# Kernel tuning notes

Measured on AMD Instinct MI355X. Metric: run time of the kernel, lower is better.

## Reference

```python
import jax, jax.numpy as jnp
import numpy as np

B, IN, COND, H, LAT, E, GH = 8192, 256, 1024, 1024, 128, 6, 64
INP = LAT + COND      # decoder layer0 input size = 1152
INTER = LAT + H       # decoder layer1/2 input size = 1152


def setup_inputs() -> dict:
    key = jax.random.key(0)
    ks = jax.random.split(key, 30)
    n = lambda k, shape, s=0.02: jax.random.normal(k, shape, dtype=jnp.float32) * s
    return {
        'x': jax.random.normal(ks[0], (B, IN), dtype=jnp.float32),
        'y': jax.random.normal(ks[1], (B, COND), dtype=jnp.float32),
        'eps': jax.random.normal(ks[2], (B, LAT), dtype=jnp.float32),
        # encoder: layer k input = prev_dim + IN (x is re-concatenated each layer)
        'enc_w0': n(ks[3], (IN + COND + IN, H)), 'enc_b0': jnp.zeros((H,), jnp.float32),
        'enc_w1': n(ks[4], (H + IN, H)),         'enc_b1': jnp.zeros((H,), jnp.float32),
        'mu_w': n(ks[5], (H, LAT)),  'mu_b': jnp.zeros((LAT,), jnp.float32),
        'lv_w': n(ks[6], (H, LAT)),  'lv_b': jnp.zeros((LAT,), jnp.float32),
        # gating network (input = latent + cond)
        'g_w0': n(ks[7], (INP, GH)), 'g_b0': jnp.zeros((GH,), jnp.float32),
        'g_w1': n(ks[8], (GH, GH)),  'g_b1': jnp.zeros((GH,), jnp.float32),
        'g_w2': n(ks[9], (GH, E)),   'g_b2': jnp.zeros((E,), jnp.float32),
        # expert weights [E, in, out] and biases [E, out] (bias init 0.01 as in source)
        'exp_w0': n(ks[10], (E, INP, H)),   'exp_b0': jnp.full((E, H), 0.01, jnp.float32),
        'exp_w1': n(ks[11], (E, INTER, H)), 'exp_b1': jnp.full((E, H), 0.01, jnp.float32),
        'exp_w2': n(ks[12], (E, INTER, IN)), 'exp_b2': jnp.full((E, IN), 0.01, jnp.float32),
    }


def _forward(x, y, eps, enc_w0, enc_b0, enc_w1, enc_b1, mu_w, mu_b, lv_w, lv_b,
             g_w0, g_b0, g_w1, g_b1, g_w2, g_b2,
             exp_w0, exp_b0, exp_w1, exp_b1, exp_w2, exp_b2):
    elu = jax.nn.elu
    # --- Encoder ---
    h = jnp.concatenate([x, y], axis=1)
    h = elu(jnp.concatenate([h, x], axis=1) @ enc_w0 + enc_b0)
    h = elu(jnp.concatenate([h, x], axis=1) @ enc_w1 + enc_b1)
    mu = h @ mu_w + mu_b
    logvar = h @ lv_w + lv_b
    # --- Reparameterize (eps passed explicitly for determinism) ---
    z = mu + eps * jnp.exp(0.5 * logvar)
    # --- MixedDecoder ---
    g = jnp.concatenate([z, y], axis=1)
    g = elu(g @ g_w0 + g_b0)
    g = elu(g @ g_w1 + g_b1)
    coeff = jax.nn.softmax(g @ g_w2 + g_b2, axis=1)  # [B, E]
    layer_out = y
    for W, bb, act in ((exp_w0, exp_b0, True), (exp_w1, exp_b1, True), (exp_w2, exp_b2, False)):
        inp = jnp.concatenate([z, layer_out], axis=1)  # [B, I]
        # fused mixture-of-experts projection: avoids materializing per-sample [B,I,O] weight
        out = coeff @ bb + jnp.einsum('be,bi,eio->bo', coeff, inp, W)
        layer_out = elu(out) if act else out
    return layer_out, mu, logvar


def reference(x, y, eps, enc_w0, enc_b0, enc_w1, enc_b1, mu_w, mu_b, lv_w, lv_b,
              g_w0, g_b0, g_w1, g_b1, g_w2, g_b2,
              exp_w0, exp_b0, exp_w1, exp_b1, exp_w2, exp_b2):
    return _forward(x, y, eps, enc_w0, enc_b0, enc_w1, enc_b1, mu_w, mu_b, lv_w, lv_b,
                    g_w0, g_b0, g_w1, g_b1, g_w2, g_b2,
                    exp_w0, exp_b0, exp_w1, exp_b1, exp_w2, exp_b2)
```

## Files before the change

### kernel.cpp

```cpp
#include <hip/hip_runtime.h>
#include <hip/hip_bf16.h>
#include <cstddef>

using u16 = unsigned short;
using short8 = __attribute__((ext_vector_type(8))) short;
using f32x4 = __attribute__((ext_vector_type(4))) float;

constexpr int B_   = 8192;
constexpr int IN_  = 256;
constexpr int COND_= 1024;
constexpr int H_   = 1024;
constexpr int LAT_ = 128;
constexpr int NE_  = 6;
constexpr int GH_  = 64;
constexpr int INP_ = 1152;
constexpr int K0_  = 1536;
constexpr int K1_  = 1280;

constexpr int BK = 64;

typedef const __attribute__((address_space(1))) void gv_t;
typedef __attribute__((address_space(3))) void lv_t;
#define GLDS(g, l) __builtin_amdgcn_global_load_lds((gv_t*)(g), (lv_t*)(l), 16, 0, 0)

__device__ __forceinline__ u16 f2b(float f) {
  __hip_bfloat16 h = __float2bfloat16(f);
  return *reinterpret_cast<u16*>(&h);
}
__device__ __forceinline__ float elu1(float x) { return x > 0.f ? x : (__expf(x) - 1.f); }

__global__ void k_transpose(const float* __restrict__ in, u16* __restrict__ out,
                            int R, int C, long inStride, long outStride) {
  __shared__ float t[32][33];
  const float* ip = in + (long)blockIdx.z * inStride;
  u16* op = out + (long)blockIdx.z * outStride;
  int c0 = blockIdx.x * 32, r0 = blockIdx.y * 32;
  int tx = threadIdx.x, ty = threadIdx.y;
#pragma unroll
  for (int i = 0; i < 4; i++) {
    int r = r0 + ty + i * 8, c = c0 + tx;
    if (r < R && c < C) t[ty + i * 8][tx] = ip[(long)r * C + c];
  }
  __syncthreads();
#pragma unroll
  for (int i = 0; i < 4; i++) {
    int c = c0 + ty + i * 8, r = r0 + tx;
    if (r < R && c < C) op[(long)c * R + r] = f2b(t[tx][ty + i * 8]);
  }
}

__global__ void k_prep(const float* __restrict__ x, const float* __restrict__ y,
                       u16* __restrict__ A0, u16* __restrict__ A1) {
  long idx = (long)blockIdx.x * blockDim.x + threadIdx.x;
  long n0 = (long)B_ * K0_;
  if (idx < n0) {
    int b = (int)(idx / K0_), c = (int)(idx % K0_);
    float v;
    if (c < IN_)            v = x[(long)b * IN_ + c];
    else if (c < IN_+COND_) v = y[(long)b * COND_ + (c - IN_)];
    else                    v = x[(long)b * IN_ + (c - IN_ - COND_)];
    A0[idx] = f2b(v);
  } else {
    long j = idx - n0;
    if (j < (long)B_ * IN_) {
      int b = (int)(j / IN_), c = (int)(j % IN_);
      A1[(long)b * K1_ + H_ + c] = f2b(x[(long)b * IN_ + c]);
    }
  }
}

__global__ void k_z(const float* __restrict__ mu, const float* __restrict__ lv,
                    const float* __restrict__ eps, const float* __restrict__ y,
                    u16* __restrict__ ZY, u16* __restrict__ D1, u16* __restrict__ D2) {
  long idx = (long)blockIdx.x * blockDim.x + threadIdx.x;
  if (idx >= (long)B_ * INP_) return;
  int b = (int)(idx / INP_), c = (int)(idx % INP_);
  if (c < LAT_) {
    long o = (long)b * LAT_ + c;
    float z = mu[o] + eps[o] * __expf(0.5f * lv[o]);
    u16 zb = f2b(z);
    ZY[idx] = zb; D1[idx] = zb; D2[idx] = zb;
  } else {
    ZY[idx] = f2b(y[(long)b * COND_ + (c - LAT_)]);
  }
}

__global__ __launch_bounds__(256) void k_gate(const float* __restrict__ G1,
    const float* __restrict__ w1, const float* __restrict__ b1,
    const float* __restrict__ w2, const float* __restrict__ b2,
    float* __restrict__ coeff) {
  __shared__ float W1[64][65];
  __shared__ float W2[64][8];
  __shared__ float B1[64], B2[8];
  int tid = threadIdx.x;
  for (int i = tid; i < 64 * 64; i += 256) W1[i >> 6][i & 63] = w1[i];
  for (int i = tid; i < 64 * 6; i += 256) W2[i / 6][i % 6] = w2[i];
  if (tid < 64) B1[tid] = b1[tid];
  if (tid < 8)  B2[tid] = (tid < 6) ? b2[tid] : 0.f;
  __syncthreads();
  int row = blockIdx.x * 256 + tid;
  const float* gr = G1 + (long)row * GH_;
  float g[64];
#pragma unroll
  for (int i = 0; i < 16; i++) {
    float4 v = *(const float4*)(gr + i * 4);
    g[i*4] = v.x; g[i*4+1] = v.y; g[i*4+2] = v.z; g[i*4+3] = v.w;
  }
  float lg[6];
#pragma unroll
  for (int e = 0; e < 6; e++) lg[e] = B2[e];
  for (int n = 0; n < 64; n++) {
    float s = B1[n];
#pragma unroll
    for (int k = 0; k < 64; k++) s += g[k] * W1[k][n];
    s = elu1(s);
#pragma unroll
    for (int e = 0; e < 6; e++) lg[e] += s * W2[n][e];
  }
  float m = lg[0];
#pragma unroll
  for (int e = 1; e < 6; e++) m = fmaxf(m, lg[e]);
  float p[6], sum = 0.f;
#pragma unroll
  for (int e = 0; e < 6; e++) { p[e] = __expf(lg[e] - m); sum += p[e]; }
  float inv = 1.f / sum;
#pragma unroll
  for (int e = 0; e < 6; e++) coeff[(long)row * 6 + e] = p[e] * inv;
}

template<int KSTEPS, int E, bool MOE>
__global__ __launch_bounds__(512, 2) void k_gemm8(
    const u16* __restrict__ A,
    const u16* __restrict__ WT,
    const float* __restrict__ bias,
    const float* __restrict__ coeff,
    int N,
    u16* __restrict__ outH, int ldo)
{
  constexpr int KK = KSTEPS * BK;
  constexpr int T = E * KSTEPS;
  __shared__ __align__(16) u16 As[3][256][BK];
  __shared__ __align__(16) u16 Bs[3][128][BK];
  __shared__ float Cf[MOE ? 256 : 1][8];

  const int tid = threadIdx.x;
  const int lane = tid & 63, w = tid >> 6;
  const int wr = w >> 1, wc = w & 1;
  const int lin = blockIdx.x + blockIdx.y * gridDim.x;
  const int rb  = (lin & 7) * 4 + ((lin >> 3) & 3);
  const int cp  = lin >> 5;
  const int brow = rb * 256, bcol = cp * 128;
  const int lr = lane & 15, hi = lane >> 4;
  const int lk = hi * 8;
  const int xsw = (lr & 7) << 3;

  if (MOE) {
    if (tid < 256) {
#pragma unroll
      for (int e2 = 0; e2 < 8; e2++)
        Cf[tid][e2] = (e2 < 6) ? coeff[(long)(brow + tid) * 6 + e2] : 0.f;
    }
    __syncthreads();
  }

  f32x4 acc[4][4];
#pragma unroll
  for (int m = 0; m < 4; m++)
#pragma unroll
    for (int n = 0; n < 4; n++)
#pragma unroll
      for (int r = 0; r < 4; r++) acc[m][n][r] = 0.f;
  f32x4 pacc[MOE ? 4 : 1][MOE ? 4 : 1];
  if constexpr (MOE) {
#pragma unroll
    for (int m = 0; m < 4; m++)
#pragma unroll
      for (int n = 0; n < 4; n++)
#pragma unroll
        for (int r = 0; r < 4; r++) pacc[m][n][r] = 0.f;
  }

  const int srow = w * 8 + (lane >> 3);
  const int sdst = (lane & 7) * 8;
  const int ssrc = ((lane & 7) ^ ((lane >> 3) & 7)) * 8;
  const u16* Asrc = A + (long)(brow + srow) * KK + ssrc;
  const u16* Bsrc = WT + (long)(bcol + srow) * KK + ssrc;

  auto STAGE = [&](int t2, int buf) {
    const int e2 = (E == 1) ? 0 : (t2 / KSTEPS);
    int k2 = (E == 1) ? t2 : (t2 % KSTEPS);
    if (E > 1 && (e2 & 1)) k2 = KSTEPS - 1 - k2;
    const u16* ap = Asrc + k2 * BK;
    const u16* bp = Bsrc + (long)e2 * ((long)N * KK) + k2 * BK;
#pragma unroll
    for (int i = 0; i < 4; i++)
      GLDS(ap + (long)(i * 64) * KK, &As[buf][i * 64 + srow][sdst]);
#pragma unroll
    for (int i = 0; i < 2; i++)
      GLDS(bp + (long)(i * 64) * KK, &Bs[buf][i * 64 + srow][sdst]);
  };

  STAGE(0, 0);
  STAGE(1, 1);

  for (int t = 0; t < T; ++t) {
    if (t + 1 < T) asm volatile("s_waitcnt vmcnt(6)" ::: "memory");
    else           asm volatile("s_waitcnt vmcnt(0)" ::: "memory");
    asm volatile("s_barrier" ::: "memory");
    if (t + 2 < T) STAGE(t + 2, (t + 2) % 3);
    const int cur = t % 3;
#pragma unroll
    for (int kk = 0; kk < BK; kk += 32) {
      short8 af[4], bfr[4];
      const int cc = (kk + lk) ^ xsw;
#pragma unroll
      for (int m = 0; m < 4; m++)
        af[m] = *(const short8*)&As[cur][wr * 64 + m * 16 + lr][cc];
#pragma unroll
      for (int n = 0; n < 4; n++)
        bfr[n] = *(const short8*)&Bs[cur][wc * 64 + n * 16 + lr][cc];
      __builtin_amdgcn_s_setprio(1);
#pragma unroll
      for (int m = 0; m < 4; m++)
#pragma unroll
        for (int n = 0; n < 4; n++) {
          if constexpr (MOE)
            pacc[m][n] = __builtin_amdgcn_mfma_f32_16x16x32_bf16(af[m], bfr[n], pacc[m][n], 0, 0, 0);
          else
            acc[m][n] = __builtin_amdgcn_mfma_f32_16x16x32_bf16(af[m], bfr[n], acc[m][n], 0, 0, 0);
        }
      __builtin_amdgcn_s_setprio(0);
    }
    if constexpr (MOE) {
      if ((t + 1) % KSTEPS == 0) {
        const int e = t / KSTEPS;
#pragma unroll
        for (int m = 0; m < 4; m++)
#pragma unroll
          for (int r = 0; r < 4; r++) {
            float c = Cf[wr * 64 + m * 16 + hi * 4 + r][e];
#pragma unroll
            for (int n = 0; n < 4; n++) acc[m][n][r] += c * pacc[m][n][r];
          }
        if (t + 1 < T) {
#pragma unroll
          for (int m = 0; m < 4; m++)
#pragma unroll
            for (int n = 0; n < 4; n++)
#pragma unroll
              for (int r = 0; r < 4; r++) pacc[m][n][r] = 0.f;
        }
      }
    }
  }

#pragma unroll
  for (int m = 0; m < 4; m++)
#pragma unroll
    for (int n = 0; n < 4; n++) {
      const int col = bcol + wc * 64 + n * 16 + lr;
#pragma unroll
      for (int r = 0; r < 4; r++) {
        const int rowl = wr * 64 + m * 16 + hi * 4 + r;
        const long row = brow + rowl;
        float v = acc[m][n][r];
        if constexpr (MOE) {
          float bv = 0.f;
#pragma unroll
          for (int e = 0; e < 6; e++) bv += Cf[rowl][e] * bias[(long)e * N + col];
          v += bv;
        } else {
          v += bias[col];
        }
        v = elu1(v);
        outH[row * (long)ldo + col] = f2b(v);
      }
    }
}

template<int MREP, bool MOE>
__global__ __launch_bounds__(256, 2) void k_gemm(
    const u16* __restrict__ A, int lda,
    const u16* __restrict__ WT, long wstride,
    const float* __restrict__ bias,
    const float* __restrict__ coeff,
    int N, int K, int E,
    u16* __restrict__ outH, float* __restrict__ outF, float* __restrict__ outF2,
    int ldo, int splitcol, const float* __restrict__ bias2, int act)
{
  constexpr int BMt = 32 * MREP;
  __shared__ __align__(16) u16 As[2][BMt][BK];
  __shared__ __align__(16) u16 Bs[2][128][BK];
  __shared__ float Cf[MOE ? BMt : 1][8];

  const int tid = threadIdx.x;
  const int lane = tid & 63, w = tid >> 6;
  const int wr = w >> 1, wc = w & 1;
  const int brow = blockIdx.x * BMt, bcol = blockIdx.y * 128;
  const int lr = lane & 15, hi = lane >> 4;
  const int lk = hi * 8;
  const int xsw = (lr & 7) << 3;

  if (MOE && tid < BMt) {
#pragma unroll
    for (int e2 = 0; e2 < 8; e2++)
      Cf[tid][e2] = (e2 < 6) ? coeff[(long)(brow + tid) * 6 + e2] : 0.f;
  }

  f32x4 acc[MREP][4];
#pragma unroll
  for (int m = 0; m < MREP; m++)
#pragma unroll
    for (int n = 0; n < 4; n++)
#pragma unroll
      for (int r = 0; r < 4; r++) acc[m][n][r] = 0.f;

  const int srow = w * 8 + (lane >> 3);
  const int sdst = (lane & 7) * 8;
  const int ssrc = ((lane & 7) ^ ((lane >> 3) & 7)) * 8;
  const u16* Asrc = A + (long)(brow + srow) * lda + ssrc;
  const u16* Bsrc = WT + (long)(bcol + srow) * K + ssrc;
  const int KSTEPS = K / BK;

  int cur = 0;
#pragma unroll
  for (int i = 0; i < BMt / 32; i++)
    GLDS(Asrc + (long)(i * 32) * lda, &As[0][i * 32 + srow][sdst]);
#pragma unroll
  for (int i = 0; i < 4; i++)
    GLDS(Bsrc + (long)(i * 32) * K, &Bs[0][i * 32 + srow][sdst]);

  for (int e = 0; e < E; ++e) {
    f32x4 pacc[MREP][4];
    if constexpr (MOE) {
#pragma unroll
      for (int m = 0; m < MREP; m++)
#pragma unroll
        for (int n = 0; n < 4; n++)
#pragma unroll
          for (int r = 0; r < 4; r++) pacc[m][n][r] = 0.f;
    }

    for (int kt = 0; kt < KSTEPS; ++kt) {
      __syncthreads();
      int ne = e, nk = kt + 1;
      if (nk == KSTEPS) { nk = 0; ne = e + 1; }
      if (ne < E) {
        const u16* ap = Asrc + (long)nk * BK;
        const u16* bp = Bsrc + (long)ne * wstride + (long)nk * BK;
#pragma unroll
        for (int i = 0; i < BMt / 32; i++)
          GLDS(ap + (long)(i * 32) * lda, &As[cur ^ 1][i * 32 + srow][sdst]);
#pragma unroll
        for (int i = 0; i < 4; i++)
          GLDS(bp + (long)(i * 32) * K, &Bs[cur ^ 1][i * 32 + srow][sdst]);
      }
#pragma unroll
      for (int kk = 0; kk < BK; kk += 32) {
        short8 af[MREP], bfr[4];
        const int cc = (kk + lk) ^ xsw;
#pragma unroll
        for (int m = 0; m < MREP; m++)
          af[m] = *(const short8*)&As[cur][wr * (16 * MREP) + m * 16 + lr][cc];
#pragma unroll
        for (int n = 0; n < 4; n++)
          bfr[n] = *(const short8*)&Bs[cur][wc * 64 + n * 16 + lr][cc];
#pragma unroll
        for (int m = 0; m < MREP; m++)
#pragma unroll
          for (int n = 0; n < 4; n++) {
            if constexpr (MOE)
              pacc[m][n] = __builtin_amdgcn_mfma_f32_16x16x32_bf16(af[m], bfr[n], pacc[m][n], 0, 0, 0);
            else
              acc[m][n] = __builtin_amdgcn_mfma_f32_16x16x32_bf16(af[m], bfr[n], acc[m][n], 0, 0, 0);
          }
      }
      cur ^= 1;
    }
    if constexpr (MOE) {
#pragma unroll
      for (int m = 0; m < MREP; m++)
#pragma unroll
        for (int r = 0; r < 4; r++) {
          float c = Cf[wr * (16 * MREP) + m * 16 + hi * 4 + r][e];
#pragma unroll
          for (int n = 0; n < 4; n++) acc[m][n][r] += c * pacc[m][n][r];
        }
    }
  }

#pragma unroll
  for (int m = 0; m < MREP; m++)
#pragma unroll
    for (int n = 0; n < 4; n++) {
      int col = bcol + wc * 64 + n * 16 + lr;
      if (col >= N) continue;
#pragma unroll
      for (int r = 0; r < 4; r++) {
        int rowl = wr * (16 * MREP) + m * 16 + hi * 4 + r;
        long row = brow + rowl;
        float v = acc[m][n][r];
        if constexpr (MOE) {
          float bv = 0.f;
#pragma unroll
          for (int e = 0; e < 6; e++) bv += Cf[rowl][e] * bias[(long)e * N + col];
          v += bv;
        } else {
          v += (col < splitcol) ? bias[col] : bias2[col - splitcol];
        }
        if (act) v = elu1(v);
        if (outH) outH[row * ldo + col] = f2b(v);
        else if (col < splitcol) outF[row * ldo + col] = v;
        else outF2[row * ldo + (col - splitcol)] = v;
      }
    }
}

extern "C" void kernel_launch(void* const* d_in, const int* in_sizes, int n_in,
                              void* d_out, int out_size, void* d_ws, size_t ws_size,
                              hipStream_t stream) {
  (void)in_sizes; (void)out_size;
  if (n_in < 23) return;
  const float* x      = (const float*)d_in[0];
  const float* y      = (const float*)d_in[1];
  const float* eps    = (const float*)d_in[2];
  const float* enc_w0 = (const float*)d_in[3];
  const float* enc_b0 = (const float*)d_in[4];
  const float* enc_w1 = (const float*)d_in[5];
  const float* enc_b1 = (const float*)d_in[6];
  const float* mu_w   = (const float*)d_in[7];
  const float* mu_b   = (const float*)d_in[8];
  const float* lv_w   = (const float*)d_in[9];
  const float* lv_b   = (const float*)d_in[10];
  const float* g_w0   = (const float*)d_in[11];
  const float* g_b0   = (const float*)d_in[12];
  const float* g_w1   = (const float*)d_in[13];
  const float* g_b1   = (const float*)d_in[14];
  const float* g_w2   = (const float*)d_in[15];
  const float* g_b2   = (const float*)d_in[16];
  const float* exp_w0 = (const float*)d_in[17];
  const float* exp_b0 = (const float*)d_in[18];
  const float* exp_w1 = (const float*)d_in[19];
  const float* exp_b1 = (const float*)d_in[20];
  const float* exp_w2 = (const float*)d_in[21];
  const float* exp_b2 = (const float*)d_in[22];

  char* ws = (char*)d_ws;
  size_t off = 0;
  auto alloc = [&](size_t bytes) -> void* {
    void* p = ws + off; off += (bytes + 255) & ~(size_t)255; return p;
  };
  u16* A0     = (u16*)alloc((size_t)B_ * K0_ * 2);
  u16* A1     = (u16*)alloc((size_t)B_ * K1_ * 2);
  u16* H2     = (u16*)alloc((size_t)B_ * H_ * 2);
  u16* ZY     = (u16*)alloc((size_t)B_ * INP_ * 2);
  u16* encw0T = (u16*)alloc((size_t)K0_ * H_ * 2);
  u16* encw1T = (u16*)alloc((size_t)K1_ * H_ * 2);
  u16* mulvT  = (u16*)alloc((size_t)256 * H_ * 2);
  u16* gw0T   = (u16*)alloc((size_t)GH_ * INP_ * 2);
  u16* ew0T   = (u16*)alloc((size_t)NE_ * H_ * INP_ * 2);
  if (ws_size < off) return;

  u16* D1 = A0;
  u16* D2 = A1;
  float* G1    = (float*)H2;
  float* COEFF = (float*)((char*)H2 + (size_t)B_ * GH_ * 4);
  u16* ew2T = (u16*)((char*)H2 + (size_t)4 * 1024 * 1024);
  u16* ew1T = ZY;

  float* outO = (float*)d_out;
  float* muO  = outO + (size_t)B_ * IN_;
  float* lvO  = muO + (size_t)B_ * LAT_;

  dim3 tb(32, 8);
  k_transpose<<<dim3(32, 48), tb, 0, stream>>>(enc_w0, encw0T, K0_, H_, 0, 0);
  k_transpose<<<dim3(32, 40), tb, 0, stream>>>(enc_w1, encw1T, K1_, H_, 0, 0);
  k_transpose<<<dim3(4, 32),  tb, 0, stream>>>(mu_w, mulvT, H_, LAT_, 0, 0);
  k_transpose<<<dim3(4, 32),  tb, 0, stream>>>(lv_w, mulvT + (size_t)LAT_ * H_, H_, LAT_, 0, 0);
  k_transpose<<<dim3(2, 36),  tb, 0, stream>>>(g_w0, gw0T, INP_, GH_, 0, 0);
  k_transpose<<<dim3(32, 36, NE_), tb, 0, stream>>>(exp_w0, ew0T, INP_, H_,
                                                    (long)INP_ * H_, (long)INP_ * H_);
  long npr = (long)B_ * K0_ + (long)B_ * IN_;
  k_prep<<<(int)((npr + 255) / 256), 256, 0, stream>>>(x, y, A0, A1);

  k_gemm8<K0_ / BK, 1, false><<<dim3(32, 8), 512, 0, stream>>>(A0, encw0T, enc_b0,
      nullptr, H_, A1, K1_);
  k_gemm8<K1_ / BK, 1, false><<<dim3(32, 8), 512, 0, stream>>>(A1, encw1T, enc_b1,
      nullptr, H_, H2, H_);
  k_gemm<2, false><<<dim3(B_ / 64, 2), 256, 0, stream>>>(H2, H_, mulvT, 0, mu_b, nullptr,
      256, H_, 1, nullptr, muO, lvO, LAT_, LAT_, lv_b, 0);

  k_transpose<<<dim3(8, 36, NE_), tb, 0, stream>>>(exp_w2, ew2T, INP_, IN_,
                                                   (long)INP_ * IN_, (long)INP_ * IN_);
  long nz = (long)B_ * INP_;
  k_z<<<(int)((nz + 255) / 256), 256, 0, stream>>>(muO, lvO, eps, y, ZY, D1, D2);

  k_gemm<2, false><<<dim3(B_ / 64, 1), 256, 0, stream>>>(ZY, INP_, gw0T, 0, g_b0, nullptr,
      GH_, INP_, 1, nullptr, G1, nullptr, GH_, GH_, nullptr, 1);
  k_gate<<<B_ / 256, 256, 0, stream>>>(G1, g_w1, g_b1, g_w2, g_b2, COEFF);

  k_gemm8<INP_ / BK, NE_, true><<<dim3(32, 8), 512, 0, stream>>>(ZY, ew0T, exp_b0,
      COEFF, H_, D1 + LAT_, INP_);
  k_transpose<<<dim3(32, 36, NE_), tb, 0, stream>>>(exp_w1, ew1T, INP_, H_,
                                                    (long)INP_ * H_, (long)INP_ * H_);
  k_gemm8<INP_ / BK, NE_, true><<<dim3(32, 8), 512, 0, stream>>>(D1, ew1T, exp_b1,
      COEFF, H_, D2 + LAT_, INP_);
  k_gemm<2, true><<<dim3(B_ / 64, 2), 256, 0, stream>>>(D2, INP_, ew2T, (long)IN_ * INP_,
      exp_b2, COEFF, IN_, INP_, NE_, nullptr, outO, nullptr, IN_, IN_, nullptr, 0);
}
```

Baseline: 639.4 us.

## Split K-tile staging into halves interleaved with MFMA phases

Restructures the GEMM main loop into two explicit half-tile phases. Each phase reads its LDS fragments, issues half of the next tile's global-to-LDS loads, then runs its MFMAs, with barriers between phases. The aim is to spread memory traffic across the compute and so hide load latency better. The cost is more barriers per iteration and fragile vmcnt accounting.

```diff
diff --git a/kernel.cpp b/kernel.cpp
--- a/kernel.cpp
+++ b/kernel.cpp
@@ -186,39 +186,38 @@
   const u16* Asrc = A + (long)(brow + srow) * KK + ssrc;
   const u16* Bsrc = WT + (long)(bcol + srow) * KK + ssrc;
 
-  auto STAGE = [&](int t2, int buf) {
+  auto STAGE_H = [&](int t2, int buf, int h) {
     const int e2 = (E == 1) ? 0 : (t2 / KSTEPS);
     int k2 = (E == 1) ? t2 : (t2 % KSTEPS);
     if (E > 1 && (e2 & 1)) k2 = KSTEPS - 1 - k2;
-    const u16* ap = Asrc + k2 * BK;
-    const u16* bp = Bsrc + (long)e2 * ((long)N * KK) + k2 * BK;
-#pragma unroll
-    for (int i = 0; i < 4; i++)
-      GLDS(ap + (long)(i * 64) * KK, &As[buf][i * 64 + srow][sdst]);
-#pragma unroll
-    for (int i = 0; i < 2; i++)
-      GLDS(bp + (long)(i * 64) * KK, &Bs[buf][i * 64 + srow][sdst]);
+    const u16* ap = Asrc + (long)k2 * BK;
+    const u16* bp = Bsrc + (long)e2 * ((long)N * KK) + (long)k2 * BK;
+    GLDS(ap + (long)((h * 2 + 0) * 64) * KK, &As[buf][(h * 2 + 0) * 64 + srow][sdst]);
+    GLDS(ap + (long)((h * 2 + 1) * 64) * KK, &As[buf][(h * 2 + 1) * 64 + srow][sdst]);
+    GLDS(bp + (long)(h * 64) * KK,           &Bs[buf][h * 64 + srow][sdst]);
   };
 
-  STAGE(0, 0);
-  STAGE(1, 1);
+  STAGE_H(0, 0, 0); STAGE_H(0, 0, 1);
+  STAGE_H(1, 1, 0); STAGE_H(1, 1, 1);
+  asm volatile("s_waitcnt vmcnt(6)" ::: "memory");
+  asm volatile("s_barrier" ::: "memory");
 
   for (int t = 0; t < T; ++t) {
-    if (t + 1 < T) asm volatile("s_waitcnt vmcnt(6)" ::: "memory");
-    else           asm volatile("s_waitcnt vmcnt(0)" ::: "memory");
-    asm volatile("s_barrier" ::: "memory");
-    if (t + 2 < T) STAGE(t + 2, (t + 2) % 3);
     const int cur = t % 3;
-#pragma unroll
-    for (int kk = 0; kk < BK; kk += 32) {
+    const int nbuf = (t + 2) % 3;
+    const bool do_stage = (t + 2 < T);
+
+    {
       short8 af[4], bfr[4];
-      const int cc = (kk + lk) ^ xsw;
+      const int cc = lk ^ xsw;
 #pragma unroll
       for (int m = 0; m < 4; m++)
         af[m] = *(const short8*)&As[cur][wr * 64 + m * 16 + lr][cc];
 #pragma unroll
       for (int n = 0; n < 4; n++)
         bfr[n] = *(const short8*)&Bs[cur][wc * 64 + n * 16 + lr][cc];
+      if (do_stage) STAGE_H(t + 2, nbuf, 0);
+      asm volatile("s_barrier" ::: "memory");
       __builtin_amdgcn_s_setprio(1);
 #pragma unroll
       for (int m = 0; m < 4; m++)
@@ -230,7 +229,38 @@
             acc[m][n] = __builtin_amdgcn_mfma_f32_16x16x32_bf16(af[m], bfr[n], acc[m][n], 0, 0, 0);
         }
       __builtin_amdgcn_s_setprio(0);
-    }
+      asm volatile("s_barrier" ::: "memory");
+    }
+
+    {
+      short8 af[4], bfr[4];
+      const int cc = (32 + lk) ^ xsw;
+#pragma unroll
+      for (int m = 0; m < 4; m++)
+        af[m] = *(const short8*)&As[cur][wr * 64 + m * 16 + lr][cc];
+#pragma unroll
+      for (int n = 0; n < 4; n++)
+        bfr[n] = *(const short8*)&Bs[cur][wc * 64 + n * 16 + lr][cc];
+      if (do_stage) STAGE_H(t + 2, nbuf, 1);
+      asm volatile("s_barrier" ::: "memory");
+      __builtin_amdgcn_s_setprio(1);
+#pragma unroll
+      for (int m = 0; m < 4; m++)
+#pragma unroll
+        for (int n = 0; n < 4; n++) {
+          if constexpr (MOE)
+            pacc[m][n] = __builtin_amdgcn_mfma_f32_16x16x32_bf16(af[m], bfr[n], pacc[m][n], 0, 0, 0);
+          else
+            acc[m][n] = __builtin_amdgcn_mfma_f32_16x16x32_bf16(af[m], bfr[n], acc[m][n], 0, 0, 0);
+        }
+      __builtin_amdgcn_s_setprio(0);
+      if (t + 1 < T) {
+        if (do_stage) asm volatile("s_waitcnt vmcnt(6)" ::: "memory");
+        else          asm volatile("s_waitcnt vmcnt(0)" ::: "memory");
+      }
+      asm volatile("s_barrier" ::: "memory");
+    }
+
     if constexpr (MOE) {
       if ((t + 1) % KSTEPS == 0) {
         const int e = t / KSTEPS;
```

New measurement: 564.5 us. 11.7% less time.

## Shrink main GEMM to 128x128 tiles with BK=32 and 4 waves

Applied to the files above, without the earlier changes.

Replaces the 256x128 tile, 8-wave, BK=64 GEMM with a 128x128 tile, 4-wave, BK=32 kernel on a 64x8 grid. The LDS swizzle becomes a 4-chunk XOR pattern. The loop is reordered so LDS fragment reads happen before the next stage's global-to-LDS loads are issued, with a single barrier per step. Smaller tiles double the block count and cut LDS use, which may raise occupancy. In exchange each block reuses loaded tiles less and needs twice as many K iterations and barriers.

```diff
diff --git a/kernel.cpp b/kernel.cpp
--- a/kernel.cpp
+++ b/kernel.cpp
@@ -129,7 +129,7 @@
 }
 
 template<int KSTEPS, int E, bool MOE>
-__global__ __launch_bounds__(512, 2) void k_gemm8(
+__global__ __launch_bounds__(256, 2) void k_g4(
     const u16* __restrict__ A,
     const u16* __restrict__ WT,
     const float* __restrict__ bias,
@@ -137,28 +137,27 @@
     int N,
     u16* __restrict__ outH, int ldo)
 {
-  constexpr int KK = KSTEPS * BK;
+  constexpr int KK = KSTEPS * 32;
   constexpr int T = E * KSTEPS;
-  __shared__ __align__(16) u16 As[3][256][BK];
-  __shared__ __align__(16) u16 Bs[3][128][BK];
-  __shared__ float Cf[MOE ? 256 : 1][8];
+  __shared__ __align__(16) u16 As[3][128][32];
+  __shared__ __align__(16) u16 Bs[3][128][32];
+  __shared__ float Cf[MOE ? 128 : 1][6];
 
   const int tid = threadIdx.x;
   const int lane = tid & 63, w = tid >> 6;
   const int wr = w >> 1, wc = w & 1;
   const int lin = blockIdx.x + blockIdx.y * gridDim.x;
-  const int rb  = (lin & 7) * 4 + ((lin >> 3) & 3);
-  const int cp  = lin >> 5;
-  const int brow = rb * 256, bcol = cp * 128;
+  const int rb  = (lin & 7) * 8 + ((lin >> 3) & 7);
+  const int cp  = lin >> 6;
+  const int brow = rb * 128, bcol = cp * 128;
   const int lr = lane & 15, hi = lane >> 4;
-  const int lk = hi * 8;
-  const int xsw = (lr & 7) << 3;
+  const int xsw3 = (lr & 3) ^ ((lr >> 2) & 3);
 
   if (MOE) {
-    if (tid < 256) {
-#pragma unroll
-      for (int e2 = 0; e2 < 8; e2++)
-        Cf[tid][e2] = (e2 < 6) ? coeff[(long)(brow + tid) * 6 + e2] : 0.f;
+    if (tid < 128) {
+#pragma unroll
+      for (int e2 = 0; e2 < 6; e2++)
+        Cf[tid][e2] = coeff[(long)(brow + tid) * 6 + e2];
     }
     __syncthreads();
   }
@@ -180,9 +179,9 @@
         for (int r = 0; r < 4; r++) pacc[m][n][r] = 0.f;
   }
 
-  const int srow = w * 8 + (lane >> 3);
-  const int sdst = (lane & 7) * 8;
-  const int ssrc = ((lane & 7) ^ ((lane >> 3) & 7)) * 8;
+  const int srow = w * 16 + (lane >> 2);
+  const int sdst = (lane & 3) * 8;
+  const int ssrc = (((lane & 3) ^ ((lane >> 2) & 3) ^ ((lane >> 4) & 3))) * 8;
   const u16* Asrc = A + (long)(brow + srow) * KK + ssrc;
   const u16* Bsrc = WT + (long)(bcol + srow) * KK + ssrc;
 
@@ -190,47 +189,47 @@
     const int e2 = (E == 1) ? 0 : (t2 / KSTEPS);
     int k2 = (E == 1) ? t2 : (t2 % KSTEPS);
     if (E > 1 && (e2 & 1)) k2 = KSTEPS - 1 - k2;
-    const u16* ap = Asrc + k2 * BK;
-    const u16* bp = Bsrc + (long)e2 * ((long)N * KK) + k2 * BK;
-#pragma unroll
-    for (int i = 0; i < 4; i++)
-      GLDS(ap + (long)(i * 64) * KK, &As[buf][i * 64 + srow][sdst]);
-#pragma unroll
-    for (int i = 0; i < 2; i++)
-      GLDS(bp + (long)(i * 64) * KK, &Bs[buf][i * 64 + srow][sdst]);
+    const u16* ap = Asrc + (long)k2 * 32;
+    const u16* bp = Bsrc + (long)e2 * ((long)N * KK) + (long)k2 * 32;
+    GLDS(ap,                  &As[buf][srow][sdst]);
+    GLDS(ap + (long)64 * KK,  &As[buf][64 + srow][sdst]);
+    GLDS(bp,                  &Bs[buf][srow][sdst]);
+    GLDS(bp + (long)64 * KK,  &Bs[buf][64 + srow][sdst]);
   };
 
   STAGE(0, 0);
   STAGE(1, 1);
+  asm volatile("s_waitcnt vmcnt(4)" ::: "memory");
+  asm volatile("s_barrier" ::: "memory");
 
   for (int t = 0; t < T; ++t) {
-    if (t + 1 < T) asm volatile("s_waitcnt vmcnt(6)" ::: "memory");
-    else           asm volatile("s_waitcnt vmcnt(0)" ::: "memory");
+    const int cur = t % 3;
+    short8 af[4], bfr[4];
+    const int cc = (hi ^ xsw3) << 3;
+#pragma unroll
+    for (int m = 0; m < 4; m++)
+      af[m] = *(const short8*)&As[cur][wr * 64 + m * 16 + lr][cc];
+#pragma unroll
+    for (int n = 0; n < 4; n++)
+      bfr[n] = *(const short8*)&Bs[cur][wc * 64 + n * 16 + lr][cc];
+    if (t + 2 < T) STAGE(t + 2, (t + 2) % 3);
+    __builtin_amdgcn_s_setprio(1);
+#pragma unroll
+    for (int m = 0; m < 4; m++)
+#pragma unroll
+      for (int n = 0; n < 4; n++) {
+        if constexpr (MOE)
+          pacc[m][n] = __builtin_amdgcn_mfma_f32_16x16x32_bf16(af[m], bfr[n], pacc[m][n], 0, 0, 0);
+        else
+          acc[m][n] = __builtin_amdgcn_mfma_f32_16x16x32_bf16(af[m], bfr[n], acc[m][n], 0, 0, 0);
+      }
+    __builtin_amdgcn_s_setprio(0);
+    if (t + 1 < T) {
+      if (t + 2 < T) asm volatile("s_waitcnt vmcnt(4)" ::: "memory");
+      else           asm volatile("s_waitcnt vmcnt(0)" ::: "memory");
+    }
     asm volatile("s_barrier" ::: "memory");
-    if (t + 2 < T) STAGE(t + 2, (t + 2) % 3);
-    const int cur = t % 3;
-#pragma unroll
-    for (int kk = 0; kk < BK; kk += 32) {
-      short8 af[4], bfr[4];
-      const int cc = (kk + lk) ^ xsw;
-#pragma unroll
-      for (int m = 0; m < 4; m++)
-        af[m] = *(const short8*)&As[cur][wr * 64 + m * 16 + lr][cc];
-#pragma unroll
-      for (int n = 0; n < 4; n++)
-        bfr[n] = *(const short8*)&Bs[cur][wc * 64 + n * 16 + lr][cc];
-      __builtin_amdgcn_s_setprio(1);
-#pragma unroll
-      for (int m = 0; m < 4; m++)
-#pragma unroll
-        for (int n = 0; n < 4; n++) {
-          if constexpr (MOE)
-            pacc[m][n] = __builtin_amdgcn_mfma_f32_16x16x32_bf16(af[m], bfr[n], pacc[m][n], 0, 0, 0);
-          else
-            acc[m][n] = __builtin_amdgcn_mfma_f32_16x16x32_bf16(af[m], bfr[n], acc[m][n], 0, 0, 0);
-        }
-      __builtin_amdgcn_s_setprio(0);
-    }
+
     if constexpr (MOE) {
       if ((t + 1) % KSTEPS == 0) {
         const int e = t / KSTEPS;
@@ -483,9 +482,9 @@
   long npr = (long)B_ * K0_ + (long)B_ * IN_;
   k_prep<<<(int)((npr + 255) / 256), 256, 0, stream>>>(x, y, A0, A1);
 
-  k_gemm8<K0_ / BK, 1, false><<<dim3(32, 8), 512, 0, stream>>>(A0, encw0T, enc_b0,
+  k_g4<K0_ / 32, 1, false><<<dim3(64, 8), 256, 0, stream>>>(A0, encw0T, enc_b0,
       nullptr, H_, A1, K1_);
-  k_gemm8<K1_ / BK, 1, false><<<dim3(32, 8), 512, 0, stream>>>(A1, encw1T, enc_b1,
+  k_g4<K1_ / 32, 1, false><<<dim3(64, 8), 256, 0, stream>>>(A1, encw1T, enc_b1,
       nullptr, H_, H2, H_);
   k_gemm<2, false><<<dim3(B_ / 64, 2), 256, 0, stream>>>(H2, H_, mulvT, 0, mu_b, nullptr,
       256, H_, 1, nullptr, muO, lvO, LAT_, LAT_, lv_b, 0);
@@ -499,11 +498,11 @@
       GH_, INP_, 1, nullptr, G1, nullptr, GH_, GH_, nullptr, 1);
   k_gate<<<B_ / 256, 256, 0, stream>>>(G1, g_w1, g_b1, g_w2, g_b2, COEFF);
 
-  k_gemm8<INP_ / BK, NE_, true><<<dim3(32, 8), 512, 0, stream>>>(ZY, ew0T, exp_b0,
+  k_g4<INP_ / 32, NE_, true><<<dim3(64, 8), 256, 0, stream>>>(ZY, ew0T, exp_b0,
       COEFF, H_, D1 + LAT_, INP_);
   k_transpose<<<dim3(32, 36, NE_), tb, 0, stream>>>(exp_w1, ew1T, INP_, H_,
                                                     (long)INP_ * H_, (long)INP_ * H_);
-  k_gemm8<INP_ / BK, NE_, true><<<dim3(32, 8), 512, 0, stream>>>(D1, ew1T, exp_b1,
+  k_g4<INP_ / 32, NE_, true><<<dim3(64, 8), 256, 0, stream>>>(D1, ew1T, exp_b1,
       COEFF, H_, D2 + LAT_, INP_);
   k_gemm<2, true><<<dim3(B_ / 64, 2), 256, 0, stream>>>(D2, INP_, ew2T, (long)IN_ * INP_,
       exp_b2, COEFF, IN_, INP_, NE_, nullptr, outO, nullptr, IN_, IN_, nullptr, 0);
```

Result: faster. 606.1 us (-5.2%).
